# Performance work log

Measured on AMD Instinct MI355X. Metric: run time of the kernel, lower is better.

The kernel has to match this reference:

```python
import jax, jax.numpy as jnp
import numpy as np

B, H, S, D = 4, 16, 2048, 128
NEG_INF = jnp.float32(-jnp.inf)


def setup_inputs() -> dict:
    key = jax.random.key(0)
    kq, kk, kv = jax.random.split(key, 3)
    q = jax.random.normal(kq, (B, H, S, D), dtype=jnp.float32)
    k = jax.random.normal(kk, (B, H, S, D), dtype=jnp.float32)
    v = jax.random.normal(kv, (B, H, S, D), dtype=jnp.float32)
    # causal mask: 1 where attention is allowed (lower triangle), 0 elsewhere
    attn_mask = jnp.tril(jnp.ones((S, S), dtype=jnp.int32))
    # padding mask: all valid (1) here; broadcasts over [B,H,S,S]
    pad_mask = jnp.ones((B, 1, 1, S), dtype=jnp.int32)
    return {"q": q, "k": k, "v": v, "attn_mask": attn_mask, "pad_mask": pad_mask}


def reference(q, k, v, attn_mask, pad_mask):
    head_size = q.shape[-1]
    scale = jnp.float32(1.0 / np.sqrt(head_size))
    # [B,H,S,S] score matrix (eager, as in the original module)
    scores = jnp.einsum("bhqd,bhkd->bhqk", q, k)
    scores = jnp.where(pad_mask == 0, NEG_INF, scores)
    scores = jnp.where(attn_mask == 0, NEG_INF, scores)
    # note: original divides by sqrt(head_size) after masking; -inf stays -inf
    attn_weights = jax.nn.softmax(scores * scale, axis=-1)
    # dropout(p=0.2) is identity at inference; omitted for a deterministic baseline
    return jnp.einsum("bhqk,bhkd->bhqd", attn_weights, v)
```

## Files before the change

kernel.cpp:

```cpp
#include <hip/hip_runtime.h>
#include <hip/hip_bf16.h>

typedef __attribute__((ext_vector_type(8))) short short8;
typedef __attribute__((ext_vector_type(4))) short short4v;
typedef __attribute__((ext_vector_type(4))) float f32x4;

constexpr int Bc = 4, Hc = 16, Sc = 2048, Dc = 128;
constexpr int QT = 64;
constexpr int KT = 64;
constexpr int QT2 = 128;
constexpr int KT2 = 32;
constexpr int TILES2 = Sc / KT2;
constexpr size_t WS_NEED = (size_t)Bc * Hc * TILES2 * 16384;
constexpr float SCALE_LOG2E = 0.08838834764831845f * 1.4426950408889634f;
constexpr float MSHIFT = 20.0f;

__device__ inline ushort bf16r(float x) {
  __hip_bfloat16 h = __float2bfloat16(x);
  return *reinterpret_cast<ushort*>(&h);
}
__device__ inline short8 pk8(f32x4 a, f32x4 b) {
  short8 t;
  #pragma unroll
  for (int j = 0; j < 4; ++j) { t[j] = (short)bf16r(a[j]); t[4 + j] = (short)bf16r(b[j]); }
  return t;
}
__device__ inline float ex2(float x) {
  float r;
  asm("v_exp_f32 %0, %1" : "=v"(r) : "v"(x));
  return r;
}
__device__ inline void gload16(const void* g, void* l) {
  __builtin_amdgcn_global_load_lds(
      (const __attribute__((address_space(1))) void*)g,
      (__attribute__((address_space(3))) void*)l, 16, 0, 0);
}

#define TRRD(dst, o) \
  asm volatile("ds_read_b64_tr_b16 %0, %1 offset:" o : "=v"(dst) : "v"(ycur))
#define TR4(T, o0, o1, o2, o3) \
  TRRD(T[0], o0); TRRD(T[1], o1); TRRD(T[2], o2); TRRD(T[3], o3);
#define WAITL4 asm volatile("s_waitcnt lgkmcnt(4)" ::: "memory"); \
  __builtin_amdgcn_sched_barrier(0)
#define WAITL0 asm volatile("s_waitcnt lgkmcnt(0)" ::: "memory"); \
  __builtin_amdgcn_sched_barrier(0)
#define MM2(dt, T) { \
  short8 b1 = __builtin_shufflevector(T[0], T[1], 0,1,2,3,4,5,6,7); \
  short8 b2 = __builtin_shufflevector(T[2], T[3], 0,1,2,3,4,5,6,7); \
  o_acc[dt] = __builtin_amdgcn_mfma_f32_16x16x32_bf16(ap1, b1, o_acc[dt], 0,0,0); \
  o_acc[dt] = __builtin_amdgcn_mfma_f32_16x16x32_bf16(ap2, b2, o_acc[dt], 0,0,0); }
#define MM4B(dt, T) { \
  short8 b1 = __builtin_shufflevector(T[0], T[1], 0,1,2,3,4,5,6,7); \
  short8 b2 = __builtin_shufflevector(T[2], T[3], 0,1,2,3,4,5,6,7); \
  oa0[dt]     = __builtin_amdgcn_mfma_f32_16x16x32_bf16(apA, b1, oa0[dt], 0,0,0); \
  oa0[dt + 1] = __builtin_amdgcn_mfma_f32_16x16x32_bf16(apA, b2, oa0[dt + 1], 0,0,0); \
  oa1[dt]     = __builtin_amdgcn_mfma_f32_16x16x32_bf16(apB, b1, oa1[dt], 0,0,0); \
  oa1[dt + 1] = __builtin_amdgcn_mfma_f32_16x16x32_bf16(apB, b2, oa1[dt + 1], 0,0,0); }

__global__ __launch_bounds__(256)
void kv_prepass(const float* __restrict__ Kg, const float* __restrict__ Vg,
                ushort* __restrict__ ws) {
  const int blk = blockIdx.x;
  const int bh = blk >> 6;
  const int tile = blk & 63;
  const int kv0 = tile * KT2;
  const int t = threadIdx.x;
  const float* Kb = Kg + (size_t)bh * Sc * Dc;
  const float* Vb = Vg + (size_t)bh * Sc * Dc;
  ushort* dst = ws + (size_t)blk * 8192;
  #pragma unroll
  for (int u = 0; u < 2; ++u) {
    const int si = t * 2 + u;
    const int sr = si >> 4;
    const int s = (si & 15) ^ (sr & 7);
    const int d0 = (s >> 2) * 32 + (s & 3) * 4;
    const float* kp = Kb + (size_t)(kv0 + sr) * Dc + d0;
    *reinterpret_cast<short8*>(dst + si * 8) =
        pk8(*reinterpret_cast<const f32x4*>(kp),
            *reinterpret_cast<const f32x4*>(kp + 16));
  }
  #pragma unroll
  for (int u = 0; u < 2; ++u) {
    const int ci = t * 2 + u;
    const int dsub = ci >> 6;
    const int rem = ci & 63;
    const int ksub = rem >> 3;
    const int kk = (rem >> 1) & 3;
    const int w = rem & 1;
    const float* vp = Vb + (size_t)(kv0 + ksub * 4 + kk) * Dc + dsub * 16 + w * 8;
    *reinterpret_cast<short8*>(dst + 4096 + ci * 8) =
        pk8(*reinterpret_cast<const f32x4*>(vp),
            *reinterpret_cast<const f32x4*>(vp + 4));
  }
}

__global__ __launch_bounds__(256, 3)
void attn_fwd_v2(const float* __restrict__ Qg, const ushort* __restrict__ ws,
                 const int* __restrict__ padg, float* __restrict__ Og) {
  const int id = blockIdx.x;
  const int qq = id >> 3;
  const int qt = 15 - (qq >> 3);
  const int bh = (id & 7) * 8 + (qq & 7);
  const int b  = bh >> 4;
  const int tid = threadIdx.x;
  const int wid = tid >> 6;
  const int lane = tid & 63;
  const int lg = lane >> 4;
  const int lr = lane & 15;

  const size_t base = (size_t)bh * Sc * Dc;
  const float* Qb = Qg + base;
  const ushort* wsb = ws + (size_t)bh * TILES2 * 8192;
  const int* padb = padg + b * Sc;

  __shared__ ushort KV[2][8192];

  const int q0a = qt * QT2 + wid * 16;
  const int q0b = q0a + 64;

  short8 aqa[4], aqb[4];
  #pragma unroll
  for (int c = 0; c < 4; ++c) {
    const float* ga = Qb + (size_t)(q0a + lr) * Dc + c * 32 + lg * 4;
    f32x4 a0 = *reinterpret_cast<const f32x4*>(ga);
    f32x4 a1 = *reinterpret_cast<const f32x4*>(ga + 16);
    const float* gb = Qb + (size_t)(q0b + lr) * Dc + c * 32 + lg * 4;
    f32x4 b0 = *reinterpret_cast<const f32x4*>(gb);
    f32x4 b1 = *reinterpret_cast<const f32x4*>(gb + 16);
    #pragma unroll
    for (int j = 0; j < 4; ++j) {
      a0[j] *= SCALE_LOG2E; a1[j] *= SCALE_LOG2E;
      b0[j] *= SCALE_LOG2E; b1[j] *= SCALE_LOG2E;
    }
    aqa[c] = pk8(a0, a1);
    aqb[c] = pk8(b0, b1);
  }

  f32x4 oa0[8], oa1[8];
  #pragma unroll
  for (int i = 0; i < 8; ++i) { oa0[i] = {0.f,0.f,0.f,0.f}; oa1[i] = {0.f,0.f,0.f,0.f}; }
  f32x4 olA = {0.f,0.f,0.f,0.f}, olB = {0.f,0.f,0.f,0.f};

  const short8 aones = { (short)0x3F80, (short)0x3F80, (short)0x3F80, (short)0x3F80,
                         (short)0x3F80, (short)0x3F80, (short)0x3F80, (short)0x3F80 };

  const uint ybase = (uint)(size_t)(&KV[0][4096]) + (uint)((lg << 7) + (lr << 3));
  const int rkey = lr & 7;
  const int ntiles = 4 * qt + 4;
  int padv_cur, padv_nxt;

  auto STAGE_ASYNC = [&](int buf, int tile) {
    const ushort* gs = wsb + (size_t)tile * 8192 + wid * 2048 + lane * 8;
    #pragma unroll
    for (int u = 0; u < 4; ++u)
      gload16(gs + u * 512, &KV[buf][wid * 2048 + u * 512]);
  };

  STAGE_ASYNC(0, 0);
  padv_cur = padb[lane & 31];
  padv_nxt = (ntiles > 1) ? padb[KT2 + (lane & 31)] : padv_cur;
  asm volatile("s_waitcnt vmcnt(0)" ::: "memory");
  __builtin_amdgcn_s_barrier();

  for (int t = 0; t < ntiles; ++t) {
    const int kv0 = t * KT2;
    const int buf = t & 1;
    const ushort* Kc = &KV[buf][0];
    const uint ycur = ybase + (uint)(buf * 16384);
    const uint pm32 = (uint)__ballot(padv_cur != 0);
    const bool active = (kv0 <= q0b + 15);

    if (t + 1 < ntiles) STAGE_ASYNC(buf ^ 1, t + 1);
    const int padv_n2 = (t + 2 < ntiles) ? padb[(t + 2) * KT2 + (lane & 31)] : 0;

    if (active) {
      f32x4 sa[2], sb[2];
      sa[0] = {0.f,0.f,0.f,0.f}; sa[1] = {0.f,0.f,0.f,0.f};
      sb[0] = {0.f,0.f,0.f,0.f}; sb[1] = {0.f,0.f,0.f,0.f};
      __builtin_amdgcn_s_setprio(1);
      #pragma unroll
      for (int c = 0; c < 4; ++c) {
        #pragma unroll
        for (int j = 0; j < 2; ++j) {
          short8 ak = *reinterpret_cast<const short8*>(
              &Kc[(j * 16 + lr) * 128 + (((c * 4 + lg) ^ rkey) << 3)]);
          sa[j] = __builtin_amdgcn_mfma_f32_16x16x32_bf16(ak, aqa[c], sa[j], 0, 0, 0);
          sb[j] = __builtin_amdgcn_mfma_f32_16x16x32_bf16(ak, aqb[c], sb[j], 0, 0, 0);
        }
      }
      __builtin_amdgcn_s_setprio(0);

      short4v ta[4], tb[4];
      TR4(ta, "0", "512", "1024", "1536");
      TR4(tb, "2048", "2560", "3072", "3584");

      const bool fullA = (kv0 + 31 <= q0a);
      const bool fullB = (kv0 + 31 <= q0b);
      const int qlimA = q0a + lr - kv0;
      const int qlimB = q0b + lr - kv0;
      f32x4 eA0, eA1, eB0, eB1;
      #pragma unroll
      for (int r = 0; r < 4; ++r) {
        const int k0 = lg * 4 + r;
        const int k1 = 16 + lg * 4 + r;
        const bool p0 = (pm32 >> k0) & 1u;
        const bool p1 = (pm32 >> k1) & 1u;
        eA0[r] = (p0 && (fullA || k0 <= qlimA)) ? ex2(sa[0][r]) : 0.f;
        eA1[r] = (p1 && (fullA || k1 <= qlimA)) ? ex2(sa[1][r]) : 0.f;
        eB0[r] = (p0 && (fullB || k0 <= qlimB)) ? ex2(sb[0][r]) : 0.f;
        eB1[r] = (p1 && (fullB || k1 <= qlimB)) ? ex2(sb[1][r]) : 0.f;
      }
      short8 apA = pk8(eA0, eA1);
      short8 apB = pk8(eB0, eB1);

      __builtin_amdgcn_s_setprio(1);
      olA = __builtin_amdgcn_mfma_f32_16x16x32_bf16(apA, aones, olA, 0, 0, 0);
      olB = __builtin_amdgcn_mfma_f32_16x16x32_bf16(apB, aones, olB, 0, 0, 0);
      WAITL4; MM4B(0, ta);
      TR4(ta, "4096", "4608", "5120", "5632");
      WAITL4; MM4B(2, tb);
      TR4(tb, "6144", "6656", "7168", "7680");
      WAITL4; MM4B(4, ta);
      WAITL0; MM4B(6, tb);
      __builtin_amdgcn_s_setprio(0);
    }

    padv_cur = padv_nxt;
    padv_nxt = padv_n2;

    asm volatile("s_waitcnt vmcnt(0)" ::: "memory");
    __builtin_amdgcn_s_barrier();
  }

  float iA[4], iB[4];
  #pragma unroll
  for (int r = 0; r < 4; ++r) { iA[r] = 1.f / olA[r]; iB[r] = 1.f / olB[r]; }
  #pragma unroll
  for (int dt = 0; dt < 8; ++dt) {
    #pragma unroll
    for (int r = 0; r < 4; ++r) {
      const int qa = q0a + lg * 4 + r;
      const int qb2 = q0b + lg * 4 + r;
      Og[base + (size_t)qa * Dc + dt * 16 + lr] = oa0[dt][r] * iA[r];
      Og[base + (size_t)qb2 * Dc + dt * 16 + lr] = oa1[dt][r] * iB[r];
    }
  }
}

__global__ __launch_bounds__(256, 2)
void attn_fwd_fb(const float* __restrict__ Qg, const float* __restrict__ Kg,
                 const float* __restrict__ Vg, const int* __restrict__ padg,
                 float* __restrict__ Og) {
  const int id = blockIdx.x;
  const int qq = id >> 3;
  const int qt = 31 - (qq >> 3);
  const int bh = (id & 7) * 8 + (qq & 7);
  const int b  = bh >> 4;
  const int tid = threadIdx.x;
  const int lane = tid & 63;
  const int lg = lane >> 4;
  const int lr = lane & 15;

  const size_t base = (size_t)bh * Sc * Dc;
  const float* Qb = Qg + base;
  const float* Kb = Kg + base;
  const float* Vb = Vg + base;
  const int* padb = padg + b * Sc;

  __shared__ ushort K_lds[2 * 8192];
  __shared__ __align__(128) ushort Y_lds[2 * 8192];

  const int q0 = qt * QT + (tid >> 6) * 16;

  short8 aqn[4];
  #pragma unroll
  for (int c = 0; c < 4; ++c) {
    const float* gq = Qb + (size_t)(q0 + lr) * Dc + c * 32 + lg * 4;
    aqn[c] = pk8(*reinterpret_cast<const f32x4*>(gq),
                 *reinterpret_cast<const f32x4*>(gq + 16));
  }

  f32x4 o_acc[8];
  #pragma unroll
  for (int i = 0; i < 8; ++i) o_acc[i] = {0.f, 0.f, 0.f, 0.f};
  f32x4 o_l = {0.f, 0.f, 0.f, 0.f};

  const short8 aones = { (short)0x3F80, (short)0x3F80, (short)0x3F80, (short)0x3F80,
                         (short)0x3F80, (short)0x3F80, (short)0x3F80, (short)0x3F80 };

  const int sr = tid >> 2;
  const int dq = tid & 3;
  const uint ybase = (uint)(size_t)(&Y_lds[0]) + (uint)((lg << 7) + (lr << 3));
  const int rkey = lr & 7;

  const int ntiles = qt + 1;
  f32x4 kreg[8], vreg[8];
  int padv_cur, padv_nxt;

  auto LOADT = [&](int kv0) {
    const float* gk = Kb + (size_t)(kv0 + sr) * Dc + dq * 32;
    const float* gv = Vb + (size_t)(kv0 + sr) * Dc + dq * 32;
    #pragma unroll
    for (int u = 0; u < 8; ++u) {
      kreg[u] = *reinterpret_cast<const f32x4*>(gk + u * 4);
      vreg[u] = *reinterpret_cast<const f32x4*>(gv + u * 4);
    }
  };
  auto STAGE = [&](int dst) {
    ushort* Kp = &K_lds[dst * 8192];
    ushort* Yp = &Y_lds[dst * 8192];
    #pragma unroll
    for (int u = 0; u < 4; ++u)
      *reinterpret_cast<short8*>(&Kp[sr * 128 + (((dq * 4 + u) ^ (sr & 7)) << 3)]) =
          pk8(kreg[u], kreg[u + 4]);
    #pragma unroll
    for (int i = 0; i < 4; ++i) {
      const int h = i >> 1, w = i & 1;
      *reinterpret_cast<short8*>(
          &Yp[(2 * dq + h) * 1024 + (sr >> 2) * 64 + (sr & 3) * 16 + w * 8]) =
          pk8(vreg[2 * i], vreg[2 * i + 1]);
    }
  };

  LOADT(0);
  padv_cur = padb[lane];
  STAGE(0);
  if (ntiles > 1) { LOADT(KT); padv_nxt = padb[KT + lane]; }
  else padv_nxt = padv_cur;
  asm volatile("s_waitcnt lgkmcnt(0)" ::: "memory");
  __builtin_amdgcn_s_barrier();

  int cur = 0;
  for (int t = 0; t < ntiles; ++t) {
    const int kv0 = t * KT;
    const ushort* Kc = &K_lds[cur * 8192];
    const uint ycur = ybase + (uint)(cur * 16384);
    const unsigned long long pmask = __ballot(padv_cur != 0);

    f32x4 sj[4];
    #pragma unroll
    for (int j = 0; j < 4; ++j) sj[j] = {0.f, 0.f, 0.f, 0.f};
    __builtin_amdgcn_s_setprio(1);
    #pragma unroll
    for (int c = 0; c < 4; ++c) {
      #pragma unroll
      for (int j = 0; j < 4; ++j) {
        short8 ak = *reinterpret_cast<const short8*>(
            &Kc[(j * 16 + lr) * 128 + (((c * 4 + lg) ^ rkey) << 3)]);
        sj[j] = __builtin_amdgcn_mfma_f32_16x16x32_bf16(ak, aqn[c], sj[j], 0, 0, 0);
      }
    }
    __builtin_amdgcn_s_setprio(0);

    short4v ta[4], tb[4];
    TR4(ta, "0", "512", "1024", "1536");
    TR4(tb, "2048", "2560", "3072", "3584");

    const bool full = (kv0 + 63 <= q0);
    f32x4 e[4];
    #pragma unroll
    for (int j = 0; j < 4; ++j) {
      #pragma unroll
      for (int r = 0; r < 4; ++r) {
        const int kil = j * 16 + lg * 4 + r;
        const bool ok = ((pmask >> kil) & 1ull) && (full || kv0 + kil <= q0 + lr);
        e[j][r] = ok ? ex2(fmaf(sj[j][r], SCALE_LOG2E, -MSHIFT)) : 0.f;
      }
    }
    short8 ap1 = pk8(e[0], e[1]);
    short8 ap2 = pk8(e[2], e[3]);

    __builtin_amdgcn_s_setprio(1);
    o_l = __builtin_amdgcn_mfma_f32_16x16x32_bf16(ap1, aones, o_l, 0, 0, 0);
    o_l = __builtin_amdgcn_mfma_f32_16x16x32_bf16(ap2, aones, o_l, 0, 0, 0);
    WAITL4; MM2(0, ta);
    TR4(ta, "4096", "4608", "5120", "5632");
    WAITL4; MM2(1, tb);
    TR4(tb, "6144", "6656", "7168", "7680");
    WAITL4; MM2(2, ta);
    TR4(ta, "8192", "8704", "9216", "9728");
    WAITL4; MM2(3, tb);
    TR4(tb, "10240", "10752", "11264", "11776");
    WAITL4; MM2(4, ta);
    TR4(ta, "12288", "12800", "13312", "13824");
    WAITL4; MM2(5, tb);
    TR4(tb, "14336", "14848", "15360", "15872");
    WAITL4; MM2(6, ta);
    WAITL0; MM2(7, tb);
    __builtin_amdgcn_s_setprio(0);

    if (t + 1 < ntiles) STAGE(cur ^ 1);
    if (t + 2 < ntiles) LOADT(kv0 + 2 * KT);
    const int padv_n2 = (t + 2 < ntiles) ? padb[kv0 + 2 * KT + lane] : 0;
    padv_cur = padv_nxt;
    padv_nxt = padv_n2;

    asm volatile("s_waitcnt lgkmcnt(0)" ::: "memory");
    __builtin_amdgcn_s_barrier();
    cur ^= 1;
  }

  float inv[4];
  #pragma unroll
  for (int r = 0; r < 4; ++r) inv[r] = 1.f / o_l[r];
  #pragma unroll
  for (int dt = 0; dt < 8; ++dt) {
    #pragma unroll
    for (int r = 0; r < 4; ++r) {
      const int qi = q0 + lg * 4 + r;
      Og[base + (size_t)qi * Dc + dt * 16 + lr] = o_acc[dt][r] * inv[r];
    }
  }
}

extern "C" void kernel_launch(void* const* d_in, const int* in_sizes, int n_in,
                              void* d_out, int out_size, void* d_ws, size_t ws_size,
                              hipStream_t stream) {
  const float* q = (const float*)d_in[0];
  const float* k = (const float*)d_in[1];
  const float* v = (const float*)d_in[2];
  const int* pad = (const int*)d_in[4];
  float* out = (float*)d_out;
  if (ws_size >= WS_NEED) {
    ushort* ws = (ushort*)d_ws;
    kv_prepass<<<dim3(Bc * Hc * TILES2), dim3(256), 0, stream>>>(k, v, ws);
    attn_fwd_v2<<<dim3(Sc / QT2 * Bc * Hc), dim3(256), 0, stream>>>(q, ws, pad, out);
  } else {
    attn_fwd_fb<<<dim3(Sc / QT * Bc * Hc), dim3(256), 0, stream>>>(q, k, v, pad, out);
  }
}
```

Baseline: 157.0 us.

## Triple-buffer KV tiles and precompute padding bitmasks in the prepass

The attention kernel now keeps three LDS buffers and prefetches tiles two steps ahead, waiting with vmcnt(4) instead of draining all loads each iteration. Padding-mask loads and per-tile ballots move into the KV prepass, which writes one 32-bit mask per tile into the workspace; the main kernel reads them with readlane. This is meant to hide global-load latency and remove per-tile pad loads, at the cost of 50% more LDS per block, which may cut occupancy. Each lane loads one mask word, so only the first 64 tiles are covered, which is exactly the tile count here.

```diff
diff --git a/kernel.cpp b/kernel.cpp
--- a/kernel.cpp
+++ b/kernel.cpp
@@ -11,7 +11,8 @@
 constexpr int QT2 = 128;
 constexpr int KT2 = 32;
 constexpr int TILES2 = Sc / KT2;
-constexpr size_t WS_NEED = (size_t)Bc * Hc * TILES2 * 16384;
+constexpr size_t WS_KV = (size_t)Bc * Hc * TILES2 * 8192;
+constexpr size_t WS_NEED = WS_KV * 2 + (size_t)Bc * TILES2 * 4 + 256;
 constexpr float SCALE_LOG2E = 0.08838834764831845f * 1.4426950408889634f;
 constexpr float MSHIFT = 20.0f;
 
@@ -59,7 +60,7 @@
 
 __global__ __launch_bounds__(256)
 void kv_prepass(const float* __restrict__ Kg, const float* __restrict__ Vg,
-                ushort* __restrict__ ws) {
+                const int* __restrict__ padg, ushort* __restrict__ ws) {
   const int blk = blockIdx.x;
   const int bh = blk >> 6;
   const int tile = blk & 63;
@@ -92,11 +93,20 @@
         pk8(*reinterpret_cast<const f32x4*>(vp),
             *reinterpret_cast<const f32x4*>(vp + 4));
   }
+  if ((bh & 15) == 0 && t < 64) {
+    const int b = bh >> 4;
+    const int pv = (t < 32) ? padg[b * Sc + kv0 + t] : 1;
+    const unsigned long long m = __ballot(pv != 0);
+    if (t == 0) {
+      uint* wm = (uint*)(ws + WS_KV);
+      wm[b * TILES2 + tile] = (uint)m;
+    }
+  }
 }
 
 __global__ __launch_bounds__(256, 3)
 void attn_fwd_v2(const float* __restrict__ Qg, const ushort* __restrict__ ws,
-                 const int* __restrict__ padg, float* __restrict__ Og) {
+                 float* __restrict__ Og) {
   const int id = blockIdx.x;
   const int qq = id >> 3;
   const int qt = 15 - (qq >> 3);
@@ -111,12 +121,13 @@
   const size_t base = (size_t)bh * Sc * Dc;
   const float* Qb = Qg + base;
   const ushort* wsb = ws + (size_t)bh * TILES2 * 8192;
-  const int* padb = padg + b * Sc;
-
-  __shared__ ushort KV[2][8192];
+
+  __shared__ ushort KV[3][8192];
 
   const int q0a = qt * QT2 + wid * 16;
   const int q0b = q0a + 64;
+
+  const uint um = ((const uint*)(ws + WS_KV))[b * TILES2 + lane];
 
   short8 aqa[4], aqb[4];
   #pragma unroll
@@ -147,7 +158,6 @@
   const uint ybase = (uint)(size_t)(&KV[0][4096]) + (uint)((lg << 7) + (lr << 3));
   const int rkey = lr & 7;
   const int ntiles = 4 * qt + 4;
-  int padv_cur, padv_nxt;
 
   auto STAGE_ASYNC = [&](int buf, int tile) {
     const ushort* gs = wsb + (size_t)tile * 8192 + wid * 2048 + lane * 8;
@@ -157,21 +167,19 @@
   };
 
   STAGE_ASYNC(0, 0);
-  padv_cur = padb[lane & 31];
-  padv_nxt = (ntiles > 1) ? padb[KT2 + (lane & 31)] : padv_cur;
   asm volatile("s_waitcnt vmcnt(0)" ::: "memory");
+  if (ntiles > 1) STAGE_ASYNC(1, 1);
   __builtin_amdgcn_s_barrier();
 
   for (int t = 0; t < ntiles; ++t) {
     const int kv0 = t * KT2;
-    const int buf = t & 1;
+    const int buf = t % 3;
     const ushort* Kc = &KV[buf][0];
     const uint ycur = ybase + (uint)(buf * 16384);
-    const uint pm32 = (uint)__ballot(padv_cur != 0);
+    const uint pm32 = (uint)__builtin_amdgcn_readlane(*(const int*)&um, t);
     const bool active = (kv0 <= q0b + 15);
 
-    if (t + 1 < ntiles) STAGE_ASYNC(buf ^ 1, t + 1);
-    const int padv_n2 = (t + 2 < ntiles) ? padb[(t + 2) * KT2 + (lane & 31)] : 0;
+    if (t + 2 < ntiles) STAGE_ASYNC((t + 2) % 3, t + 2);
 
     if (active) {
       f32x4 sa[2], sb[2];
@@ -225,10 +233,7 @@
       __builtin_amdgcn_s_setprio(0);
     }
 
-    padv_cur = padv_nxt;
-    padv_nxt = padv_n2;
-
-    asm volatile("s_waitcnt vmcnt(0)" ::: "memory");
+    asm volatile("s_waitcnt vmcnt(4)" ::: "memory");
     __builtin_amdgcn_s_barrier();
   }
 
@@ -423,8 +428,8 @@
   float* out = (float*)d_out;
   if (ws_size >= WS_NEED) {
     ushort* ws = (ushort*)d_ws;
-    kv_prepass<<<dim3(Bc * Hc * TILES2), dim3(256), 0, stream>>>(k, v, ws);
-    attn_fwd_v2<<<dim3(Sc / QT2 * Bc * Hc), dim3(256), 0, stream>>>(q, ws, pad, out);
+    kv_prepass<<<dim3(Bc * Hc * TILES2), dim3(256), 0, stream>>>(k, v, pad, ws);
+    attn_fwd_v2<<<dim3(Sc / QT2 * Bc * Hc), dim3(256), 0, stream>>>(q, ws, out);
   } else {
     attn_fwd_fb<<<dim3(Sc / QT * Bc * Hc), dim3(256), 0, stream>>>(q, k, v, pad, out);
   }
```

Result: faster. 137.3 us (-12.6%).
